# Kernel optimization log

Measured on AMD Instinct MI355X. Metric: run time of the kernel, lower is better.

The kernel has to match this reference:

```python
import jax, jax.numpy as jnp
import numpy as np

ALPHAS = (0.1, 0.3, 0.6)
WEIGHTS = (0.5, 0.3, 0.2)
HUBER_MARGIN = 1.0
B, S = 2048, 8192


def setup_inputs() -> dict:
    key = jax.random.key(0)
    k1, k2 = jax.random.split(key)
    pred = jax.random.normal(k1, (B, S), dtype=jnp.float32)
    target = jax.random.normal(k2, (B, S), dtype=jnp.float32)
    return {"pred": pred, "target": target}


def _ema(x, alpha):
    # x: [B, S]; ema[0] = x[0]; ema[i] = alpha*x[i] + (1-alpha)*ema[i-1]
    x0 = x[:, 0]
    def step(carry, xi):
        nc = alpha * xi + (1.0 - alpha) * carry
        return nc, nc
    _, ys = jax.lax.scan(step, x0, x[:, 1:].T)  # ys: [S-1, B]
    return jnp.concatenate([x0[:, None], ys.T], axis=1)  # [B, S]


def _huber_loss(pred_delta, target_delta):
    dir_agreement = pred_delta * target_delta
    step_err = jnp.abs(pred_delta - target_delta)
    quad = jnp.square(jnp.maximum(HUBER_MARGIN - dir_agreement, 0.0)) / (2.0 * HUBER_MARGIN)
    return jnp.where(dir_agreement < 0, step_err, quad).mean(axis=1)  # [B]


def reference(pred, target):
    loss = jnp.zeros((pred.shape[0],), dtype=pred.dtype)
    for alpha, weight in zip(ALPHAS, WEIGHTS):
        pe = _ema(pred, alpha)
        te = _ema(target, alpha)
        pd = pe[:, 1:] - pe[:, :-1]
        td = te[:, 1:] - te[:, :-1]
        loss = loss + weight * _huber_loss(pd, td)
    return loss.mean()  # reduction='mean'
```

## Files before the change

### kernel.cpp

```cpp
#include <hip/hip_runtime.h>

#define B_ROWS 2048
#define S_LEN  8192
#define PER_LANE 16
#define TPB 512
#define WPB 8
#define CHUNK (64 * PER_LANE)
#define NBLOCKS B_ROWS

constexpr double cpowi(double b, int e) { double r = 1.0; for (int i = 0; i < e; ++i) r *= b; return r; }
constexpr float tof(double x) { return (x < 1.2e-38 && x > -1.2e-38) ? 0.0f : (float)x; }

#define W0f 0.9f
#define W1f 0.7f
#define W2f 0.4f
#define IA0 10.0f
#define IA1 (1.0f / 0.3f)
#define IA2 (1.0f / 0.6f)
#define SE0 0.2f
#define SE1 0.6f
#define SE2 1.2f
constexpr float NA0 = -(0.1f * 0.1f);
constexpr float NA1 = -(0.3f * 0.3f);
constexpr float NA2 = -(0.6f * 0.6f);

constexpr float D0_1 = tof(cpowi(0.9, 16)),  D0_2 = tof(cpowi(0.9, 32));
constexpr float D0_4 = tof(cpowi(0.9, 64)),  D0_8 = tof(cpowi(0.9, 128));
constexpr float D1_1 = tof(cpowi(0.7, 16)),  D1_2 = tof(cpowi(0.7, 32));
constexpr float D2_1 = tof(cpowi(0.4, 16));

#define L2_0 (-0.15200309344504997f)
#define L2_1 (-0.51457317282975830f)
#define L2_2 (-1.32192809488736230f)

__device__ __forceinline__ float scan4(float v, int lane, float d1, float d2, float d4, float d8) {
    float u;
    u = __shfl_up(v, 1); v += (lane >= 1 ? d1 : 0.0f) * u;
    u = __shfl_up(v, 2); v += (lane >= 2 ? d2 : 0.0f) * u;
    u = __shfl_up(v, 4); v += (lane >= 4 ? d4 : 0.0f) * u;
    u = __shfl_up(v, 8); v += (lane >= 8 ? d8 : 0.0f) * u;
    return v;
}
__device__ __forceinline__ float scan2(float v, int lane, float d1, float d2) {
    float u;
    u = __shfl_up(v, 1); v += (lane >= 1 ? d1 : 0.0f) * u;
    u = __shfl_up(v, 2); v += (lane >= 2 ? d2 : 0.0f) * u;
    return v;
}
__device__ __forceinline__ float scan1(float v, int lane, float d1) {
    float u;
    u = __shfl_up(v, 1); v += (lane >= 1 ? d1 : 0.0f) * u;
    return v;
}

__global__ void __launch_bounds__(TPB, 8) msl_main(const float* __restrict__ pred,
                                                   const float* __restrict__ targ,
                                                   float* __restrict__ partial) {
    const int lane = threadIdx.x & 63;
    const int wave = threadIdx.x >> 6;
    const float* __restrict__ prow = pred + (size_t)blockIdx.x * S_LEN;
    const float* __restrict__ trow = targ + (size_t)blockIdx.x * S_LEN;
    const int base = wave * CHUNK + lane * PER_LANE;

    float xp[PER_LANE], xt[PER_LANE];
    const float4* p4 = reinterpret_cast<const float4*>(prow + base);
    const float4* t4 = reinterpret_cast<const float4*>(trow + base);
#pragma unroll
    for (int j = 0; j < PER_LANE / 4; ++j) {
        float4 a = p4[j];
        float4 b = t4[j];
        xp[4 * j + 0] = a.x; xp[4 * j + 1] = a.y; xp[4 * j + 2] = a.z; xp[4 * j + 3] = a.w;
        xt[4 * j + 0] = b.x; xt[4 * j + 1] = b.y; xt[4 * j + 2] = b.z; xt[4 * j + 3] = b.w;
    }
#pragma unroll
    for (int j = 0; j < PER_LANE; ++j) {
        asm volatile("" : "+v"(xp[j]), "+v"(xt[j]));
    }

    const bool w0   = (wave == 0);
    const bool lz   = (lane == 0);
    const bool head = w0 && lz;

    float Mp0 = head ? xp[0] * IA0 : 0.0f;
    float Mp1 = head ? xp[0] * IA1 : 0.0f;
    float Mp2 = head ? xp[0] * IA2 : 0.0f;
    float Mt0 = head ? xt[0] * IA0 : 0.0f;
    float Mt1 = head ? xt[0] * IA1 : 0.0f;
    float Mt2 = head ? xt[0] * IA2 : 0.0f;
#pragma unroll
    for (int j = 0; j < PER_LANE; ++j) {
        Mp0 = fmaf(W0f, Mp0, xp[j]);
        Mp1 = fmaf(W1f, Mp1, xp[j]);
        Mp2 = fmaf(W2f, Mp2, xp[j]);
        Mt0 = fmaf(W0f, Mt0, xt[j]);
        Mt1 = fmaf(W1f, Mt1, xt[j]);
        Mt2 = fmaf(W2f, Mt2, xt[j]);
    }

    float vp0 = scan4(Mp0, lane, D0_1, D0_2, D0_4, D0_8);
    float vp1 = scan2(Mp1, lane, D1_1, D1_2);
    float vp2 = scan1(Mp2, lane, D2_1);
    float vt0 = scan4(Mt0, lane, D0_1, D0_2, D0_4, D0_8);
    float vt1 = scan2(Mt1, lane, D1_1, D1_2);
    float vt2 = scan1(Mt2, lane, D2_1);

    __shared__ float sex[WPB][6];
    if (lane == 63) {
        sex[wave][0] = vp0; sex[wave][1] = vp1; sex[wave][2] = vp2;
        sex[wave][3] = vt0; sex[wave][4] = vt1; sex[wave][5] = vt2;
    }
    __syncthreads();

    float Cp0 = 0.f, Cp1 = 0.f, Cp2 = 0.f, Ct0 = 0.f, Ct1 = 0.f, Ct2 = 0.f;
    if (wave > 0) {
        Cp0 = sex[wave - 1][0]; Cp1 = sex[wave - 1][1]; Cp2 = sex[wave - 1][2];
        Ct0 = sex[wave - 1][3]; Ct1 = sex[wave - 1][4]; Ct2 = sex[wave - 1][5];
    }

    const float e  = (float)(PER_LANE * lane);
    const float G0 = exp2f(e * L2_0);
    const float G1 = exp2f(e * L2_1);
    const float G2 = exp2f(e * L2_2);

    float up0 = __shfl_up(vp0, 1), up1 = __shfl_up(vp1, 1), up2 = __shfl_up(vp2, 1);
    float ut0 = __shfl_up(vt0, 1), ut1 = __shfl_up(vt1, 1), ut2 = __shfl_up(vt2, 1);

    float yp0 = lz ? (w0 ? xp[0] * IA0 : Cp0) : fmaf(G0, Cp0, up0);
    float yp1 = lz ? (w0 ? xp[0] * IA1 : Cp1) : fmaf(G1, Cp1, up1);
    float yp2 = lz ? (w0 ? xp[0] * IA2 : Cp2) : fmaf(G2, Cp2, up2);
    float yt0 = lz ? (w0 ? xt[0] * IA0 : Ct0) : fmaf(G0, Ct0, ut0);
    float yt1 = lz ? (w0 ? xt[0] * IA1 : Ct1) : fmaf(G1, Ct1, ut1);
    float yt2 = lz ? (w0 ? xt[0] * IA2 : Ct2) : fmaf(G2, Ct2, ut2);

    float acc0 = 0.f, acc1 = 0.f, acc2 = 0.f;
    const float skip = head ? 0.0f : 1.0f;
#pragma unroll
    for (int j = 0; j < PER_LANE; ++j) {
        float n, dup0, dut0, dup1, dut1, dup2, dut2;
        n = fmaf(W0f, yp0, xp[j]); dup0 = n - yp0; yp0 = n;
        n = fmaf(W0f, yt0, xt[j]); dut0 = n - yt0; yt0 = n;
        n = fmaf(W1f, yp1, xp[j]); dup1 = n - yp1; yp1 = n;
        n = fmaf(W1f, yt1, xt[j]); dut1 = n - yt1; yt1 = n;
        n = fmaf(W2f, yp2, xp[j]); dup2 = n - yp2; yp2 = n;
        n = fmaf(W2f, yt2, xt[j]); dut2 = n - yt2; yt2 = n;

        float m0 = dup0 * dut0, m1 = dup1 * dut1, m2 = dup2 * dut2;
        float se0 = SE0 * fabsf(dup0 - dut0);
        float se1 = SE1 * fabsf(dup1 - dut1);
        float se2 = SE2 * fabsf(dup2 - dut2);
        float mm0 = fmaxf(fmaf(NA0, m0, 1.0f), 0.0f);
        float mm1 = fmaxf(fmaf(NA1, m1, 1.0f), 0.0f);
        float mm2 = fmaxf(fmaf(NA2, m2, 1.0f), 0.0f);
        float h0 = (m0 < 0.0f) ? se0 : mm0 * mm0;
        float h1 = (m1 < 0.0f) ? se1 : mm1 * mm1;
        float h2 = (m2 < 0.0f) ? se2 : mm2 * mm2;
        if (j == 0) { h0 *= skip; h1 *= skip; h2 *= skip; }
        acc0 += h0; acc1 += h1; acc2 += h2;
    }

    float wacc = 0.25f * acc0 + 0.15f * acc1 + 0.10f * acc2;
#pragma unroll
    for (int o = 32; o > 0; o >>= 1) wacc += __shfl_down(wacc, o);

    __shared__ float sred[WPB];
    if (lz) sred[wave] = wacc;
    __syncthreads();
    if (threadIdx.x == 0) {
        float s = 0.f;
#pragma unroll
        for (int i = 0; i < WPB; ++i) s += sred[i];
        partial[blockIdx.x] = s;
    }
}

__global__ void __launch_bounds__(256) msl_reduce(const float* __restrict__ partial,
                                                  float* __restrict__ out) {
    const int tid = threadIdx.x;
    float v = 0.f;
#pragma unroll
    for (int k = 0; k < NBLOCKS / 256; ++k) v += partial[tid + 256 * k];
#pragma unroll
    for (int o = 32; o > 0; o >>= 1) v += __shfl_down(v, o);
    __shared__ float s[4];
    if ((tid & 63) == 0) s[tid >> 6] = v;
    __syncthreads();
    if (tid == 0)
        out[0] = (s[0] + s[1] + s[2] + s[3]) *
                 (float)(1.0 / ((double)(S_LEN - 1) * (double)B_ROWS));
}

extern "C" void kernel_launch(void* const* d_in, const int* in_sizes, int n_in,
                              void* d_out, int out_size, void* d_ws, size_t ws_size,
                              hipStream_t stream) {
    const float* pred = (const float*)d_in[0];
    const float* targ = (const float*)d_in[1];
    float* out = (float*)d_out;
    float* partial = (float*)d_ws;

    msl_main<<<NBLOCKS, TPB, 0, stream>>>(pred, targ, partial);
    msl_reduce<<<1, 256, 0, stream>>>(partial, out);
}
```

Before: 146.6 us.

## Scan EMA of input differences directly and stage deltas in LDS

Reformulates the recurrence so each lane scans a scaled EMA of the input differences (dx), whose value at each step is directly the delta term. This removes the per-step subtraction and the head initialization with inverse alphas. The dx values are written to shared memory (64 KB per block) during the first pass and re-read in the second pass instead of being kept in registers. Launch bounds drop from 8 to 4 blocks per CU to fit the LDS, so occupancy falls and extra LDS traffic is added in exchange for lower register pressure.

```diff
diff --git a/kernel.cpp b/kernel.cpp
--- a/kernel.cpp
+++ b/kernel.cpp
@@ -14,9 +14,6 @@
 #define W0f 0.9f
 #define W1f 0.7f
 #define W2f 0.4f
-#define IA0 10.0f
-#define IA1 (1.0f / 0.3f)
-#define IA2 (1.0f / 0.6f)
 #define SE0 0.2f
 #define SE1 0.6f
 #define SE2 1.2f
@@ -53,7 +50,7 @@
     return v;
 }
 
-__global__ void __launch_bounds__(TPB, 8) msl_main(const float* __restrict__ pred,
+__global__ void __launch_bounds__(TPB, 4) msl_main(const float* __restrict__ pred,
                                                    const float* __restrict__ targ,
                                                    float* __restrict__ partial) {
     const int lane = threadIdx.x & 63;
@@ -62,39 +59,50 @@
     const float* __restrict__ trow = targ + (size_t)blockIdx.x * S_LEN;
     const int base = wave * CHUNK + lane * PER_LANE;
 
+    __shared__ float dxs[WPB][2][PER_LANE][64];
+    __shared__ float sex[WPB][6];
+    __shared__ float sred[WPB];
+
+    const bool w0 = (wave == 0);
+    const bool lz = (lane == 0);
+
+    float pv0p = 0.f, pv0t = 0.f;
+    if (lz && wave > 0) { pv0p = prow[base - 1]; pv0t = trow[base - 1]; }
+
     float xp[PER_LANE], xt[PER_LANE];
-    const float4* p4 = reinterpret_cast<const float4*>(prow + base);
-    const float4* t4 = reinterpret_cast<const float4*>(trow + base);
-#pragma unroll
-    for (int j = 0; j < PER_LANE / 4; ++j) {
-        float4 a = p4[j];
-        float4 b = t4[j];
-        xp[4 * j + 0] = a.x; xp[4 * j + 1] = a.y; xp[4 * j + 2] = a.z; xp[4 * j + 3] = a.w;
-        xt[4 * j + 0] = b.x; xt[4 * j + 1] = b.y; xt[4 * j + 2] = b.z; xt[4 * j + 3] = b.w;
-    }
+    {
+        const float4* p4 = reinterpret_cast<const float4*>(prow + base);
+        const float4* t4 = reinterpret_cast<const float4*>(trow + base);
+#pragma unroll
+        for (int j = 0; j < PER_LANE / 4; ++j) {
+            float4 a = p4[j];
+            float4 b = t4[j];
+            xp[4 * j + 0] = a.x; xp[4 * j + 1] = a.y; xp[4 * j + 2] = a.z; xp[4 * j + 3] = a.w;
+            xt[4 * j + 0] = b.x; xt[4 * j + 1] = b.y; xt[4 * j + 2] = b.z; xt[4 * j + 3] = b.w;
+        }
+    }
+
+    float pvp = __shfl_up(xp[PER_LANE - 1], 1);
+    float pvt = __shfl_up(xt[PER_LANE - 1], 1);
+    if (lz) {
+        pvp = w0 ? xp[0] : pv0p;
+        pvt = w0 ? xt[0] : pv0t;
+    }
+
+    float Mp0 = 0.f, Mp1 = 0.f, Mp2 = 0.f, Mt0 = 0.f, Mt1 = 0.f, Mt2 = 0.f;
+    float prevp = pvp, prevt = pvt;
 #pragma unroll
     for (int j = 0; j < PER_LANE; ++j) {
-        asm volatile("" : "+v"(xp[j]), "+v"(xt[j]));
-    }
-
-    const bool w0   = (wave == 0);
-    const bool lz   = (lane == 0);
-    const bool head = w0 && lz;
-
-    float Mp0 = head ? xp[0] * IA0 : 0.0f;
-    float Mp1 = head ? xp[0] * IA1 : 0.0f;
-    float Mp2 = head ? xp[0] * IA2 : 0.0f;
-    float Mt0 = head ? xt[0] * IA0 : 0.0f;
-    float Mt1 = head ? xt[0] * IA1 : 0.0f;
-    float Mt2 = head ? xt[0] * IA2 : 0.0f;
-#pragma unroll
-    for (int j = 0; j < PER_LANE; ++j) {
-        Mp0 = fmaf(W0f, Mp0, xp[j]);
-        Mp1 = fmaf(W1f, Mp1, xp[j]);
-        Mp2 = fmaf(W2f, Mp2, xp[j]);
-        Mt0 = fmaf(W0f, Mt0, xt[j]);
-        Mt1 = fmaf(W1f, Mt1, xt[j]);
-        Mt2 = fmaf(W2f, Mt2, xt[j]);
+        float dxp = xp[j] - prevp; prevp = xp[j];
+        float dxt = xt[j] - prevt; prevt = xt[j];
+        dxs[wave][0][j][lane] = dxp;
+        dxs[wave][1][j][lane] = dxt;
+        Mp0 = fmaf(W0f, Mp0, dxp);
+        Mp1 = fmaf(W1f, Mp1, dxp);
+        Mp2 = fmaf(W2f, Mp2, dxp);
+        Mt0 = fmaf(W0f, Mt0, dxt);
+        Mt1 = fmaf(W1f, Mt1, dxt);
+        Mt2 = fmaf(W2f, Mt2, dxt);
     }
 
     float vp0 = scan4(Mp0, lane, D0_1, D0_2, D0_4, D0_8);
@@ -104,7 +112,6 @@
     float vt1 = scan2(Mt1, lane, D1_1, D1_2);
     float vt2 = scan1(Mt2, lane, D2_1);
 
-    __shared__ float sex[WPB][6];
     if (lane == 63) {
         sex[wave][0] = vp0; sex[wave][1] = vp1; sex[wave][2] = vp2;
         sex[wave][3] = vt0; sex[wave][4] = vt1; sex[wave][5] = vt2;
@@ -125,29 +132,30 @@
     float up0 = __shfl_up(vp0, 1), up1 = __shfl_up(vp1, 1), up2 = __shfl_up(vp2, 1);
     float ut0 = __shfl_up(vt0, 1), ut1 = __shfl_up(vt1, 1), ut2 = __shfl_up(vt2, 1);
 
-    float yp0 = lz ? (w0 ? xp[0] * IA0 : Cp0) : fmaf(G0, Cp0, up0);
-    float yp1 = lz ? (w0 ? xp[0] * IA1 : Cp1) : fmaf(G1, Cp1, up1);
-    float yp2 = lz ? (w0 ? xp[0] * IA2 : Cp2) : fmaf(G2, Cp2, up2);
-    float yt0 = lz ? (w0 ? xt[0] * IA0 : Ct0) : fmaf(G0, Ct0, ut0);
-    float yt1 = lz ? (w0 ? xt[0] * IA1 : Ct1) : fmaf(G1, Ct1, ut1);
-    float yt2 = lz ? (w0 ? xt[0] * IA2 : Ct2) : fmaf(G2, Ct2, ut2);
+    float yp0 = lz ? (w0 ? 0.0f : Cp0) : fmaf(G0, Cp0, up0);
+    float yp1 = lz ? (w0 ? 0.0f : Cp1) : fmaf(G1, Cp1, up1);
+    float yp2 = lz ? (w0 ? 0.0f : Cp2) : fmaf(G2, Cp2, up2);
+    float yt0 = lz ? (w0 ? 0.0f : Ct0) : fmaf(G0, Ct0, ut0);
+    float yt1 = lz ? (w0 ? 0.0f : Ct1) : fmaf(G1, Ct1, ut1);
+    float yt2 = lz ? (w0 ? 0.0f : Ct2) : fmaf(G2, Ct2, ut2);
 
     float acc0 = 0.f, acc1 = 0.f, acc2 = 0.f;
-    const float skip = head ? 0.0f : 1.0f;
+    const float skip = (w0 && lz) ? 0.0f : 1.0f;
 #pragma unroll
     for (int j = 0; j < PER_LANE; ++j) {
-        float n, dup0, dut0, dup1, dut1, dup2, dut2;
-        n = fmaf(W0f, yp0, xp[j]); dup0 = n - yp0; yp0 = n;
-        n = fmaf(W0f, yt0, xt[j]); dut0 = n - yt0; yt0 = n;
-        n = fmaf(W1f, yp1, xp[j]); dup1 = n - yp1; yp1 = n;
-        n = fmaf(W1f, yt1, xt[j]); dut1 = n - yt1; yt1 = n;
-        n = fmaf(W2f, yp2, xp[j]); dup2 = n - yp2; yp2 = n;
-        n = fmaf(W2f, yt2, xt[j]); dut2 = n - yt2; yt2 = n;
-
-        float m0 = dup0 * dut0, m1 = dup1 * dut1, m2 = dup2 * dut2;
-        float se0 = SE0 * fabsf(dup0 - dut0);
-        float se1 = SE1 * fabsf(dup1 - dut1);
-        float se2 = SE2 * fabsf(dup2 - dut2);
+        float dxp = dxs[wave][0][j][lane];
+        float dxt = dxs[wave][1][j][lane];
+        yp0 = fmaf(W0f, yp0, dxp);
+        yt0 = fmaf(W0f, yt0, dxt);
+        yp1 = fmaf(W1f, yp1, dxp);
+        yt1 = fmaf(W1f, yt1, dxt);
+        yp2 = fmaf(W2f, yp2, dxp);
+        yt2 = fmaf(W2f, yt2, dxt);
+
+        float m0 = yp0 * yt0, m1 = yp1 * yt1, m2 = yp2 * yt2;
+        float se0 = SE0 * fabsf(yp0 - yt0);
+        float se1 = SE1 * fabsf(yp1 - yt1);
+        float se2 = SE2 * fabsf(yp2 - yt2);
         float mm0 = fmaxf(fmaf(NA0, m0, 1.0f), 0.0f);
         float mm1 = fmaxf(fmaf(NA1, m1, 1.0f), 0.0f);
         float mm2 = fmaxf(fmaf(NA2, m2, 1.0f), 0.0f);
@@ -162,7 +170,6 @@
 #pragma unroll
     for (int o = 32; o > 0; o >>= 1) wacc += __shfl_down(wacc, o);
 
-    __shared__ float sred[WPB];
     if (lz) sred[wave] = wacc;
     __syncthreads();
     if (threadIdx.x == 0) {
```

New measurement: 143.9 us. Within noise of the previous version (-1.8%).
